# Kernel optimization log

Hardware: AMD Instinct MI355X
Metric: run time of the kernel (lower is better)

## Reference

```python
import jax, jax.numpy as jnp
import numpy as np

B, S, D = 1, 2048, 4096
H, KV = 32, 8
HD = D // H          # 128
N_REP = H // KV      # 4
ROPE_THETA = 10000.0


def setup_inputs() -> dict:
    key = jax.random.key(0)
    ks = jax.random.split(key, 5)
    x = jax.random.normal(ks[0], (B, S, D), dtype=jnp.float32)
    wq = jax.random.normal(ks[1], (H * HD, D), dtype=jnp.float32) * 0.02
    wk = jax.random.normal(ks[2], (KV * HD, D), dtype=jnp.float32) * 0.02
    wv = jax.random.normal(ks[3], (KV * HD, D), dtype=jnp.float32) * 0.02
    wo = jax.random.normal(ks[4], (D, H * HD), dtype=jnp.float32) * 0.02
    # precomputed RoPE frequencies: freqs_cis = exp(i * t * theta_j)
    inv_freq = 1.0 / (ROPE_THETA ** (np.arange(0, HD, 2, dtype=np.float32) / HD))  # [HD/2]
    angles = np.arange(S, dtype=np.float32)[:, None] * inv_freq[None, :]           # [S, HD/2]
    freqs_cos = jnp.asarray(np.cos(angles))
    freqs_sin = jnp.asarray(np.sin(angles))
    return {"x": x, "freqs_cos": freqs_cos, "freqs_sin": freqs_sin,
            "wq": wq, "wk": wk, "wv": wv, "wo": wo}


def _rope(t, cos, sin):
    # t: [B,S,h,HD]; even/odd interleaved pairs form complex numbers
    tr, ti = t[..., 0::2], t[..., 1::2]                 # [B,S,h,HD/2]
    cos = cos[None, :, None, :]
    sin = sin[None, :, None, :]
    out = jnp.stack([tr * cos - ti * sin, tr * sin + ti * cos], axis=-1)
    return out.reshape(t.shape)


def reference(x, freqs_cos, freqs_sin, wq, wk, wv, wo):
    bs, seqlen, _ = x.shape
    xq = jnp.einsum('bsd,ed->bse', x, wq).reshape(bs, seqlen, H, HD)
    xk = jnp.einsum('bsd,ed->bse', x, wk).reshape(bs, seqlen, KV, HD)
    xv = jnp.einsum('bsd,ed->bse', x, wv).reshape(bs, seqlen, KV, HD)
    xq = _rope(xq, freqs_cos, freqs_sin)
    xk = _rope(xk, freqs_cos, freqs_sin)
    # repeat_kv: GQA expand kv heads by n_rep
    keys = jnp.repeat(xk, N_REP, axis=2)    # [B,S,H,HD]
    values = jnp.repeat(xv, N_REP, axis=2)
    scale = 1.0 / np.sqrt(HD).astype(np.float32)
    scores = jnp.einsum('bshd,bthd->bhst', xq, keys) * scale  # [B,H,S,S]
    causal = jnp.tril(jnp.ones((seqlen, seqlen), dtype=bool))
    scores = jnp.where(causal[None, None], scores, jnp.finfo(scores.dtype).min)
    attn = jax.nn.softmax(scores, axis=-1)
    out = jnp.einsum('bhst,bthd->bshd', attn, values).reshape(bs, seqlen, H * HD)
    return jnp.einsum('bse,de->bsd', out, wo)
```

## Files before the change

### kernel.cpp

```cpp
#include <hip/hip_runtime.h>
#include <hip/hip_bf16.h>
#include <stdint.h>

#define SEQ   2048
#define DM    4096
#define NH    32
#define NKV   8
#define HD    128
#define DKV   1024

typedef __attribute__((ext_vector_type(8))) short bf8_t;
typedef __attribute__((ext_vector_type(4))) float f4_t;
typedef __attribute__((ext_vector_type(16))) float f16x;

__device__ __forceinline__ short f2bf(float f) {
  union { float f; uint32_t u; } v; v.f = f;
  uint32_t r = v.u + 0x7FFFu + ((v.u >> 16) & 1u);
  return (short)(r >> 16);
}
__device__ __forceinline__ float bf2f(short s) {
  union { uint32_t u; float f; } v; v.u = ((uint32_t)(uint16_t)s) << 16;
  return v.f;
}
__device__ __forceinline__ uint32_t cvtpk(float lo, float hi) {
  uint32_t r;
  asm("v_cvt_pk_bf16_f32 %0, %1, %2" : "=v"(r) : "v"(lo), "v"(hi));
  return r;
}

__device__ __forceinline__ void async_copy16(const void* gsrc, void* ldst) {
  auto g = reinterpret_cast<const __attribute__((address_space(1))) uint32_t*>(
      reinterpret_cast<uintptr_t>(gsrc));
  auto l = reinterpret_cast<__attribute__((address_space(3))) uint32_t*>(
      reinterpret_cast<uintptr_t>(ldst));
  __builtin_amdgcn_global_load_lds(g, l, 16, 0, 0);
}

__device__ __forceinline__ f4_t mfma16(bf8_t a, bf8_t b, f4_t c) {
  return __builtin_amdgcn_mfma_f32_16x16x32_bf16(a, b, c, 0, 0, 0);
}
__device__ __forceinline__ f16x mfma32(bf8_t a, bf8_t b, f16x c) {
  return __builtin_amdgcn_mfma_f32_32x32x16_bf16(a, b, c, 0, 0, 0);
}

template<int N> __device__ __forceinline__ void vmwait();
template<> __device__ __forceinline__ void vmwait<3>() {
  asm volatile("s_waitcnt vmcnt(3)" ::: "memory");
}
template<> __device__ __forceinline__ void vmwait<4>() {
  asm volatile("s_waitcnt vmcnt(4)" ::: "memory");
}

union U4B8 { uint32_t w[4]; bf8_t v; };

__global__ void cvt_all_kernel(const float* __restrict__ x,
                               const float* __restrict__ wq,
                               const float* __restrict__ wk,
                               const float* __restrict__ wv,
                               const float* __restrict__ wo,
                               short* __restrict__ out)
{
  const int E0 = SEQ * DM / 4;
  const int E1 = E0 + DM * DM / 4;
  const int E2 = E1 + DKV * DM / 4;
  const int E3 = E2 + DKV * DM / 4;
  const int E4 = E3 + DM * DM / 4;
  const int stride = gridDim.x * blockDim.x;
  for (int i = blockIdx.x * blockDim.x + threadIdx.x; i < E4; i += stride) {
    const float4* src; int off;
    if (i < E0)      { src = (const float4*)x;  off = i; }
    else if (i < E1) { src = (const float4*)wq; off = i - E0; }
    else if (i < E2) { src = (const float4*)wk; off = i - E1; }
    else if (i < E3) { src = (const float4*)wv; off = i - E2; }
    else             { src = (const float4*)wo; off = i - E3; }
    float4 v = src[off];
    short4 o;
    o.x = f2bf(v.x); o.y = f2bf(v.y); o.z = f2bf(v.z); o.w = f2bf(v.w);
    ((short4*)out)[i] = o;
  }
}

template<int MODE, int BM, int BN>
__global__ __launch_bounds__(512, 2)
void gemm8_kernel(const short* __restrict__ A,
                  const short* __restrict__ Bw,
                  float* __restrict__ Cf,
                  short* __restrict__ Cq,
                  short* __restrict__ Ck,
                  short* __restrict__ Cv)
{
  constexpr int MREP = BM / 32;
  constexpr int SB   = BN / 64;
  constexpr int SPP  = (SB == 4) ? 2 : (MREP / 4);
  constexpr int AJ   = BM / 128;
  constexpr int NT   = DM / 64;

  __shared__ short As[2][BM * 64];
  __shared__ short Bs[2][BN * 64];

  const int tid = threadIdx.x, lane = tid & 63, wid = tid >> 6;
  const int wr = wid >> 2, wn = wid & 3;
  const int cl = lane & 15, kh = lane >> 4;
  const int row0 = blockIdx.y * BM;
  const int col0 = blockIdx.x * BN;

  f4_t acc[MREP][SB];
  #pragma unroll
  for (int i = 0; i < MREP; i++)
    #pragma unroll
    for (int j = 0; j < SB; j++) { acc[i][j][0]=0.f; acc[i][j][1]=0.f; acc[i][j][2]=0.f; acc[i][j][3]=0.f; }

  auto STGA = [&](short* T, int h, int kt) {
    #pragma unroll
    for (int j = 0; j < AJ; ++j) {
      const int c = wid * (64 * AJ) + j * 64 + lane;
      const int row = h * (BM / 2) + (c >> 3), pcol = c & 7;
      const int lcol = pcol ^ (row & 7);
      async_copy16(&A[(size_t)(row0 + row) * DM + kt * 64 + lcol * 8],
                   &T[(h * (BM * 4) + c) * 8]);
    }
  };
  auto STGB = [&](short* T, int sl, int kt) {
    const int c = wid * 64 + lane;
    const int row = sl * 64 + (c >> 3), pcol = c & 7;
    const int lcol = pcol ^ (row & 7);
    async_copy16(&Bw[(size_t)(col0 + row) * DM + kt * 64 + lcol * 8],
                 &T[(sl * 512 + c) * 8]);
  };

  bf8_t bF[SB][2];
  bf8_t aF[SPP][2];
  auto LDA = [&](const short* T, int ms0) {
    #pragma unroll
    for (int s = 0; s < SPP; ++s)
      #pragma unroll
      for (int q = 0; q < 2; ++q) {
        const int row = wr * (BM / 2) + (ms0 + s) * 16 + cl;
        const int pcol = (q * 4 + kh) ^ (row & 7);
        aF[s][q] = *(const bf8_t*)&T[(row * 8 + pcol) * 8];
      }
  };
  auto LDB = [&](const short* T) {
    #pragma unroll
    for (int n = 0; n < SB; ++n)
      #pragma unroll
      for (int q = 0; q < 2; ++q) {
        const int row = wn * (16 * SB) + n * 16 + cl;
        const int pcol = (q * 4 + kh) ^ (row & 7);
        bF[n][q] = *(const bf8_t*)&T[(row * 8 + pcol) * 8];
      }
  };

#define PHASE(TA, TB, PH, READB, STGSTMT, VMC)                                \
  {                                                                           \
    LDA(TA, (PH) * SPP);                                                      \
    if (READB) LDB(TB);                                                       \
    STGSTMT                                                                   \
    __builtin_amdgcn_s_barrier();                                             \
    asm volatile("s_waitcnt lgkmcnt(0)" ::: "memory");                        \
    __builtin_amdgcn_s_setprio(1);                                            \
    _Pragma("unroll")                                                         \
    for (int s_ = 0; s_ < SPP; ++s_) {                                        \
      _Pragma("unroll")                                                       \
      for (int n_ = 0; n_ < SB; ++n_) {                                       \
        _Pragma("unroll")                                                     \
        for (int q_ = 0; q_ < 2; ++q_)                                        \
          acc[(PH) * SPP + s_][n_] =                                          \
              mfma16(aF[s_][q_], bF[n_][q_], acc[(PH) * SPP + s_][n_]);       \
      }                                                                       \
    }                                                                         \
    __builtin_amdgcn_s_setprio(0);                                            \
    if (VMC) vmwait<SB>();                                                    \
    __builtin_amdgcn_s_barrier();                                             \
  }

  #pragma unroll
  for (int sl = 0; sl < SB; ++sl) STGB(Bs[0], sl, 0);
  STGA(As[0], 0, 0); STGA(As[0], 1, 0);
  #pragma unroll
  for (int sl = 0; sl < SB; ++sl) STGB(Bs[1], sl, 1);
  vmwait<SB>();
  __builtin_amdgcn_s_barrier();

  for (int i = 0; i < NT / 2; ++i) {
    const int tA1 = 2 * i + 1;
    int t2 = 2 * i + 2; if (t2 > NT - 1) t2 = NT - 1;
    int t3 = 2 * i + 3; if (t3 > NT - 1) t3 = NT - 1;
    if constexpr (SB == 4) {
      PHASE(As[0], Bs[0], 0, true,  { STGA(As[1], 0, tA1); STGA(As[1], 1, tA1); }, false);
      PHASE(As[0], Bs[0], 1, false, { STGB(Bs[0], 0, t2); STGB(Bs[0], 1, t2);
                                      STGB(Bs[0], 2, t2); STGB(Bs[0], 3, t2); }, true);
      PHASE(As[1], Bs[1], 0, true,  { STGA(As[0], 0, t2); STGA(As[0], 1, t2); }, false);
      PHASE(As[1], Bs[1], 1, false, { STGB(Bs[1], 0, t3); STGB(Bs[1], 1, t3);
                                      STGB(Bs[1], 2, t3); STGB(Bs[1], 3, t3); }, true);
    } else {
      PHASE(As[0], Bs[0], 0, true,  { STGA(As[1], 0, tA1); STGA(As[1], 1, tA1); }, false);
      PHASE(As[0], Bs[0], 1, false, { STGB(Bs[0], 0, t2); }, false);
      PHASE(As[0], Bs[0], 2, false, { STGB(Bs[0], 1, t2); }, false);
      PHASE(As[0], Bs[0], 3, false, { STGB(Bs[0], 2, t2); }, true);
      PHASE(As[1], Bs[1], 0, true,  { STGA(As[0], 0, t2); STGA(As[0], 1, t2); }, false);
      PHASE(As[1], Bs[1], 1, false, { STGB(Bs[1], 0, t3); }, false);
      PHASE(As[1], Bs[1], 2, false, { STGB(Bs[1], 1, t3); }, false);
      PHASE(As[1], Bs[1], 3, false, { STGB(Bs[1], 2, t3); }, true);
    }
  }
#undef PHASE

  const int rb = kh * 4;
  #pragma unroll
  for (int mi = 0; mi < MREP; mi++) {
    const int m0 = row0 + wr * (BM / 2) + mi * 16 + rb;
    #pragma unroll
    for (int ni = 0; ni < SB; ni++) {
      const int n = col0 + wn * (16 * SB) + ni * 16 + cl;
      if (MODE == 0) {
        #pragma unroll
        for (int r = 0; r < 4; r++) Cf[(size_t)(m0 + r) * DM + n] = acc[mi][ni][r];
      } else if (n < DM) {
        #pragma unroll
        for (int r = 0; r < 4; r++) Cq[(size_t)(m0 + r) * DM + n] = f2bf(acc[mi][ni][r]);
      } else if (n < DM + DKV) {
        const int nk = n - DM;
        #pragma unroll
        for (int r = 0; r < 4; r++) Ck[(size_t)(m0 + r) * DKV + nk] = f2bf(acc[mi][ni][r]);
      } else {
        const int nv = n - DM - DKV;
        short4 pk;
        pk.x = f2bf(acc[mi][ni][0]); pk.y = f2bf(acc[mi][ni][1]);
        pk.z = f2bf(acc[mi][ni][2]); pk.w = f2bf(acc[mi][ni][3]);
        *(short4*)&Cv[(size_t)nv * SEQ + m0] = pk;
      }
    }
  }
}

__global__ void rope_kernel(short* __restrict__ Qb, short* __restrict__ Kb,
                            const float* __restrict__ fcos, const float* __restrict__ fsin)
{
  const int NQG = SEQ * (DM / 8);
  const int NKG = SEQ * (DKV / 8);
  int idx = blockIdx.x * blockDim.x + threadIdx.x;
  if (idx >= NQG + NKG) return;
  short* T; int s, g, row8;
  if (idx < NQG) { T = Qb; s = idx >> 9; g = idx & 511; row8 = DM / 8; }
  else { int j = idx - NQG; T = Kb; s = j >> 7; g = j & 127; row8 = DKV / 8; }
  const int i0 = (g & 15) * 4;
  const float4 cv = *(const float4*)&fcos[s * 64 + i0];
  const float4 sv = *(const float4*)&fsin[s * 64 + i0];
  short* ptr = T + (size_t)s * (row8 * 8) + g * 8;
  U4B8 v = *(U4B8*)ptr;
  U4B8 o;
  {
    const float e0 = bf2f((short)(v.w[0] & 0xFFFF)), o0 = bf2f((short)(v.w[0] >> 16));
    o.w[0] = cvtpk(e0 * cv.x - o0 * sv.x, e0 * sv.x + o0 * cv.x);
    const float e1 = bf2f((short)(v.w[1] & 0xFFFF)), o1 = bf2f((short)(v.w[1] >> 16));
    o.w[1] = cvtpk(e1 * cv.y - o1 * sv.y, e1 * sv.y + o1 * cv.y);
    const float e2 = bf2f((short)(v.w[2] & 0xFFFF)), o2 = bf2f((short)(v.w[2] >> 16));
    o.w[2] = cvtpk(e2 * cv.z - o2 * sv.z, e2 * sv.z + o2 * cv.z);
    const float e3 = bf2f((short)(v.w[3] & 0xFFFF)), o3 = bf2f((short)(v.w[3] >> 16));
    o.w[3] = cvtpk(e3 * cv.w - o3 * sv.w, e3 * sv.w + o3 * cv.w);
  }
  *(U4B8*)ptr = o;
}

__device__ __forceinline__ void flash_stage(const short* __restrict__ Kb,
                                            const short* __restrict__ Vt,
                                            short* Kl, short* Vl,
                                            int kv0, int hkv, int wid, int lane)
{
  #pragma unroll
  for (int i = 0; i < 4; ++i) {
    int c = wid * 256 + i * 64 + lane;
    int row = c >> 4, pos = c & 15;
    int dc = pos ^ (row & 7);
    async_copy16(&Kb[(size_t)(kv0 + row) * DKV + hkv * HD + dc * 8], &Kl[c * 8]);
  }
  #pragma unroll
  for (int i = 0; i < 4; ++i) {
    int c = wid * 256 + i * 64 + lane;
    int row = c >> 3, pos = c & 7;
    int kc = pos ^ (row & 7);
    async_copy16(&Vt[(size_t)(hkv * HD + row) * SEQ + kv0 + kc * 8], &Vl[c * 8]);
  }
}

__device__ __forceinline__ void flash_compute(const short* __restrict__ Kl,
                                              const short* __restrict__ Vl,
                                              const bf8_t* qF, f16x* accO,
                                              float& m_run, float& l_run,
                                              int kv0, int qw0, int c31, int hi)
{
  const float scale = 0.08838834764831845f;

  f16x accS[2];
  #pragma unroll
  for (int nu = 0; nu < 2; ++nu) {
    #pragma unroll
    for (int r = 0; r < 16; ++r) accS[nu][r] = 0.f;
  }
  #pragma unroll
  for (int nu = 0; nu < 2; ++nu) {
    const int row = nu * 32 + c31, rx = row & 7;
    #pragma unroll
    for (int s = 0; s < 8; ++s) {
      const int pos = (2 * s + hi) ^ rx;
      bf8_t kf = *(const bf8_t*)&Kl[row * 128 + pos * 8];
      accS[nu] = mfma32(kf, qF[s], accS[nu]);
    }
  }

  if (kv0 + 63 > qw0) {
    const int q_abs = qw0 + c31;
    #pragma unroll
    for (int nu = 0; nu < 2; ++nu)
      #pragma unroll
      for (int r = 0; r < 16; ++r) {
        const int kv_abs = kv0 + 32 * nu + (r & 3) + 8 * (r >> 2) + 4 * hi;
        if (kv_abs > q_abs) accS[nu][r] = -3.0e38f;
      }
  }

  float rm = -3.0e38f;
  #pragma unroll
  for (int nu = 0; nu < 2; ++nu)
    #pragma unroll
    for (int r = 0; r < 16; ++r) rm = fmaxf(rm, accS[nu][r]);
  rm = fmaxf(rm, __shfl_xor(rm, 32));
  const float pmax = rm * scale;
  if (!__all(pmax - m_run <= 8.0f)) {
    const float mnew = fmaxf(m_run, pmax);
    const float corr = __expf(m_run - mnew);
    m_run = mnew;
    l_run *= corr;
    #pragma unroll
    for (int dt = 0; dt < 4; ++dt)
      #pragma unroll
      for (int r = 0; r < 16; ++r) accO[dt][r] *= corr;
  }

  float tsum = 0.f;
  uint32_t u[8][2];
  #pragma unroll
  for (int m = 0; m < 8; ++m) {
    const int nu = m >> 2, rb = 4 * (m & 3);
    float p0 = __expf(fmaf(accS[nu][rb + 0], scale, -m_run));
    float p1 = __expf(fmaf(accS[nu][rb + 1], scale, -m_run));
    float p2 = __expf(fmaf(accS[nu][rb + 2], scale, -m_run));
    float p3 = __expf(fmaf(accS[nu][rb + 3], scale, -m_run));
    tsum += (p0 + p1) + (p2 + p3);
    u[m][0] = cvtpk(p0, p1);
    u[m][1] = cvtpk(p2, p3);
  }
  l_run += tsum + __shfl_xor(tsum, 32);

  bf8_t pa[4];
  #pragma unroll
  for (int ks = 0; ks < 4; ++ks) {
    const uint32_t a0 = u[2 * ks][0],     a1 = u[2 * ks][1];
    const uint32_t b0 = u[2 * ks + 1][0], b1 = u[2 * ks + 1][1];
    const uint32_t mp0 = hi ? a0 : b0, mp1 = hi ? a1 : b1;
    const uint32_t s0 = __shfl_xor(mp0, 32), s1 = __shfl_xor(mp1, 32);
    U4B8 f;
    f.w[0] = hi ? s0 : a0;
    f.w[1] = hi ? s1 : a1;
    f.w[2] = hi ? b0 : s0;
    f.w[3] = hi ? b1 : s1;
    pa[ks] = f.v;
  }

  #pragma unroll
  for (int dt = 0; dt < 4; ++dt) {
    const int row = dt * 32 + c31, rx = row & 7;
    #pragma unroll
    for (int ks = 0; ks < 4; ++ks) {
      const int pos = (2 * ks + hi) ^ rx;
      bf8_t vf = *(const bf8_t*)&Vl[row * 64 + pos * 8];
      accO[dt] = mfma32(vf, pa[ks], accO[dt]);
    }
  }
}

__global__ __launch_bounds__(256, 2)
void flash_kernel(const short* __restrict__ Qb,
                  const short* __restrict__ Kb,
                  const short* __restrict__ Vt,
                  short* __restrict__ Ob)
{
  __shared__ short Kl0[64 * 128], Kl1[64 * 128];
  __shared__ short Vl0[128 * 64], Vl1[128 * 64];

  const int tid = threadIdx.x, lane = tid & 63, wid = tid >> 6;
  const int c31 = lane & 31, hi = lane >> 5;

  const int b = blockIdx.x;
  const int pairid = b & 255, halfsel = b >> 8;
  const int h = pairid >> 3, p = pairid & 7;
  const int qt = halfsel ? (15 - p) : p;
  const int q0 = qt * 128;
  const int hkv = h >> 2;
  const int qw0 = q0 + wid * 32;

  bf8_t qF[8];
  {
    const size_t qb = (size_t)(qw0 + c31) * DM + h * HD + hi * 8;
    #pragma unroll
    for (int s = 0; s < 8; ++s) qF[s] = *(const bf8_t*)&Qb[qb + s * 16];
  }

  f16x accO[4];
  #pragma unroll
  for (int dt = 0; dt < 4; ++dt)
    #pragma unroll
    for (int r = 0; r < 16; ++r) accO[dt][r] = 0.f;
  float m_run = -INFINITY, l_run = 0.f;

  const int nt = (q0 >> 6) + 2;

  flash_stage(Kb, Vt, Kl0, Vl0, 0, hkv, wid, lane);
  __syncthreads();
  for (int t = 0; t < nt; t += 2) {
    flash_stage(Kb, Vt, Kl1, Vl1, (t + 1) * 64, hkv, wid, lane);
    if (t * 64 <= qw0 + 31)
      flash_compute(Kl0, Vl0, qF, accO, m_run, l_run, t * 64, qw0, c31, hi);
    __syncthreads();
    if (t + 2 < nt) flash_stage(Kb, Vt, Kl0, Vl0, (t + 2) * 64, hkv, wid, lane);
    if ((t + 1) * 64 <= qw0 + 31)
      flash_compute(Kl1, Vl1, qF, accO, m_run, l_run, (t + 1) * 64, qw0, c31, hi);
    __syncthreads();
  }

  short* Ol = (wid < 2) ? &Kl0[wid * 4096] : &Kl1[(wid - 2) * 4096];
  const float oinv = 1.0f / l_run;
  #pragma unroll
  for (int dt = 0; dt < 4; ++dt)
    #pragma unroll
    for (int w = 0; w < 8; ++w) {
      const int r = 2 * w;
      const int d0 = (r & 3) + 8 * (r >> 2) + 4 * hi + dt * 32;
      const uint32_t pk = cvtpk(accO[dt][r] * oinv, accO[dt][r + 1] * oinv);
      const int pos = (d0 >> 3) ^ (c31 & 7);
      *(uint32_t*)&Ol[c31 * 128 + pos * 8 + (d0 & 7)] = pk;
    }
  __syncthreads();
  const int rowq = lane >> 1;
  #pragma unroll
  for (int i = 0; i < 8; ++i) {
    const int dc = (lane & 1) * 8 + i;
    const int pos = dc ^ (rowq & 7);
    int4 v = *(const int4*)&Ol[rowq * 128 + pos * 8];
    *(int4*)&Ob[(size_t)(q0 + wid * 32 + rowq) * DM + h * HD + dc * 8] = v;
  }
}

extern "C" void kernel_launch(void* const* d_in, const int* in_sizes, int n_in,
                              void* d_out, int out_size, void* d_ws, size_t ws_size,
                              hipStream_t stream)
{
  const float* x    = (const float*)d_in[0];
  const float* fcos = (const float*)d_in[1];
  const float* fsin = (const float*)d_in[2];
  const float* wq   = (const float*)d_in[3];
  const float* wk   = (const float*)d_in[4];
  const float* wv   = (const float*)d_in[5];
  const float* wo   = (const float*)d_in[6];
  float* out = (float*)d_out;

  char* p = (char*)d_ws;
  short* xb  = (short*)p; p += (size_t)SEQ * DM * 2;
  short* wqb = (short*)p; p += (size_t)DM * DM * 2;
  short* wkb = (short*)p; p += (size_t)DKV * DM * 2;
  short* wvb = (short*)p; p += (size_t)DKV * DM * 2;
  short* wob = (short*)p; p += (size_t)DM * DM * 2;
  short* Qb  = (short*)p; p += (size_t)SEQ * DM * 2;
  short* Kb  = (short*)p; p += (size_t)SEQ * DKV * 2;
  short* Vt  = (short*)p; p += (size_t)DKV * SEQ * 2;
  short* Ab  = (short*)p; p += (size_t)SEQ * DM * 2;
  (void)wkb; (void)wvb;

  cvt_all_kernel<<<2048, 256, 0, stream>>>(x, wq, wk, wv, wo, xb);

  gemm8_kernel<1, 256, 192><<<dim3(32, 8), 512, 0, stream>>>(xb, wqb,
                                                             nullptr, Qb, Kb, Vt);
  rope_kernel<<<5120, 256, 0, stream>>>(Qb, Kb, fcos, fsin);
  flash_kernel<<<512, 256, 0, stream>>>(Qb, Kb, Vt, Ab);
  gemm8_kernel<0, 128, 256><<<dim3(16, 16), 512, 0, stream>>>(Ab, wob,
                                                              out, nullptr, nullptr, nullptr);
}
```

Before: 275.9 us.

## Fuse Q RoPE into flash Q-fragment load and simplify GEMM phase schedule

The flash kernel now applies RoPE to Q as it loads the Q fragments into registers, reading cos/sin directly. The standalone rope kernel shrinks to handle K only, which removes a full read and write pass over the Q buffer. Separately, the GEMM main loop is unified to two compute phases per buffer with SPP = MREP/2. For the QKV GEMM configuration (BN=192) this halves the number of phases and barriers but puts more MFMAs and loads in each phase, which may hurt load/compute interleaving.

```diff
diff --git a/kernel.cpp b/kernel.cpp
--- a/kernel.cpp
+++ b/kernel.cpp
@@ -91,7 +91,7 @@
 {
   constexpr int MREP = BM / 32;
   constexpr int SB   = BN / 64;
-  constexpr int SPP  = (SB == 4) ? 2 : (MREP / 4);
+  constexpr int SPP  = MREP / 2;
   constexpr int AJ   = BM / 128;
   constexpr int NT   = DM / 64;
 
@@ -183,26 +183,17 @@
   __builtin_amdgcn_s_barrier();
 
   for (int i = 0; i < NT / 2; ++i) {
-    const int tA1 = 2 * i + 1;
+    const int t1 = 2 * i + 1;
     int t2 = 2 * i + 2; if (t2 > NT - 1) t2 = NT - 1;
     int t3 = 2 * i + 3; if (t3 > NT - 1) t3 = NT - 1;
-    if constexpr (SB == 4) {
-      PHASE(As[0], Bs[0], 0, true,  { STGA(As[1], 0, tA1); STGA(As[1], 1, tA1); }, false);
-      PHASE(As[0], Bs[0], 1, false, { STGB(Bs[0], 0, t2); STGB(Bs[0], 1, t2);
-                                      STGB(Bs[0], 2, t2); STGB(Bs[0], 3, t2); }, true);
-      PHASE(As[1], Bs[1], 0, true,  { STGA(As[0], 0, t2); STGA(As[0], 1, t2); }, false);
-      PHASE(As[1], Bs[1], 1, false, { STGB(Bs[1], 0, t3); STGB(Bs[1], 1, t3);
-                                      STGB(Bs[1], 2, t3); STGB(Bs[1], 3, t3); }, true);
-    } else {
-      PHASE(As[0], Bs[0], 0, true,  { STGA(As[1], 0, tA1); STGA(As[1], 1, tA1); }, false);
-      PHASE(As[0], Bs[0], 1, false, { STGB(Bs[0], 0, t2); }, false);
-      PHASE(As[0], Bs[0], 2, false, { STGB(Bs[0], 1, t2); }, false);
-      PHASE(As[0], Bs[0], 3, false, { STGB(Bs[0], 2, t2); }, true);
-      PHASE(As[1], Bs[1], 0, true,  { STGA(As[0], 0, t2); STGA(As[0], 1, t2); }, false);
-      PHASE(As[1], Bs[1], 1, false, { STGB(Bs[1], 0, t3); }, false);
-      PHASE(As[1], Bs[1], 2, false, { STGB(Bs[1], 1, t3); }, false);
-      PHASE(As[1], Bs[1], 3, false, { STGB(Bs[1], 2, t3); }, true);
-    }
+    PHASE(As[0], Bs[0], 0, true,
+          { STGA(As[1], 0, t1); STGA(As[1], 1, t1); }, false);
+    PHASE(As[0], Bs[0], 1, false,
+          { _Pragma("unroll") for (int sl = 0; sl < SB; ++sl) STGB(Bs[0], sl, t2); }, true);
+    PHASE(As[1], Bs[1], 0, true,
+          { STGA(As[0], 0, t2); STGA(As[0], 1, t2); }, false);
+    PHASE(As[1], Bs[1], 1, false,
+          { _Pragma("unroll") for (int sl = 0; sl < SB; ++sl) STGB(Bs[1], sl, t3); }, true);
   }
 #undef PHASE
 
@@ -234,20 +225,17 @@
   }
 }
 
-__global__ void rope_kernel(short* __restrict__ Qb, short* __restrict__ Kb,
-                            const float* __restrict__ fcos, const float* __restrict__ fsin)
-{
-  const int NQG = SEQ * (DM / 8);
+__global__ void rope_k_kernel(short* __restrict__ Kb,
+                              const float* __restrict__ fcos, const float* __restrict__ fsin)
+{
   const int NKG = SEQ * (DKV / 8);
   int idx = blockIdx.x * blockDim.x + threadIdx.x;
-  if (idx >= NQG + NKG) return;
-  short* T; int s, g, row8;
-  if (idx < NQG) { T = Qb; s = idx >> 9; g = idx & 511; row8 = DM / 8; }
-  else { int j = idx - NQG; T = Kb; s = j >> 7; g = j & 127; row8 = DKV / 8; }
+  if (idx >= NKG) return;
+  const int s = idx >> 7, g = idx & 127;
   const int i0 = (g & 15) * 4;
   const float4 cv = *(const float4*)&fcos[s * 64 + i0];
   const float4 sv = *(const float4*)&fsin[s * 64 + i0];
-  short* ptr = T + (size_t)s * (row8 * 8) + g * 8;
+  short* ptr = Kb + (size_t)s * DKV + g * 8;
   U4B8 v = *(U4B8*)ptr;
   U4B8 o;
   {
@@ -384,6 +372,8 @@
 void flash_kernel(const short* __restrict__ Qb,
                   const short* __restrict__ Kb,
                   const short* __restrict__ Vt,
+                  const float* __restrict__ fcos,
+                  const float* __restrict__ fsin,
                   short* __restrict__ Ob)
 {
   __shared__ short Kl0[64 * 128], Kl1[64 * 128];
@@ -402,9 +392,27 @@
 
   bf8_t qF[8];
   {
-    const size_t qb = (size_t)(qw0 + c31) * DM + h * HD + hi * 8;
-    #pragma unroll
-    for (int s = 0; s < 8; ++s) qF[s] = *(const bf8_t*)&Qb[qb + s * 16];
+    const int qrow = qw0 + c31;
+    const size_t qb = (size_t)qrow * DM + h * HD + hi * 8;
+    const int tb = qrow * 64 + hi * 4;
+    #pragma unroll
+    for (int s = 0; s < 8; ++s) {
+      U4B8 v; v.v = *(const bf8_t*)&Qb[qb + s * 16];
+      const float4 cv = *(const float4*)&fcos[tb + s * 8];
+      const float4 sv = *(const float4*)&fsin[tb + s * 8];
+      U4B8 o;
+      {
+        const float e0 = bf2f((short)(v.w[0] & 0xFFFF)), d0 = bf2f((short)(v.w[0] >> 16));
+        o.w[0] = cvtpk(e0 * cv.x - d0 * sv.x, e0 * sv.x + d0 * cv.x);
+        const float e1 = bf2f((short)(v.w[1] & 0xFFFF)), d1 = bf2f((short)(v.w[1] >> 16));
+        o.w[1] = cvtpk(e1 * cv.y - d1 * sv.y, e1 * sv.y + d1 * cv.y);
+        const float e2 = bf2f((short)(v.w[2] & 0xFFFF)), d2 = bf2f((short)(v.w[2] >> 16));
+        o.w[2] = cvtpk(e2 * cv.z - d2 * sv.z, e2 * sv.z + d2 * cv.z);
+        const float e3 = bf2f((short)(v.w[3] & 0xFFFF)), d3 = bf2f((short)(v.w[3] >> 16));
+        o.w[3] = cvtpk(e3 * cv.w - d3 * sv.w, e3 * sv.w + d3 * cv.w);
+      }
+      qF[s] = o.v;
+    }
   }
 
   f16x accO[4];
@@ -481,8 +489,8 @@
 
   gemm8_kernel<1, 256, 192><<<dim3(32, 8), 512, 0, stream>>>(xb, wqb,
                                                              nullptr, Qb, Kb, Vt);
-  rope_kernel<<<5120, 256, 0, stream>>>(Qb, Kb, fcos, fsin);
-  flash_kernel<<<512, 256, 0, stream>>>(Qb, Kb, Vt, Ab);
+  rope_k_kernel<<<1024, 256, 0, stream>>>(Kb, fcos, fsin);
+  flash_kernel<<<512, 256, 0, stream>>>(Qb, Kb, Vt, fcos, fsin, Ab);
   gemm8_kernel<0, 128, 256><<<dim3(16, 16), 512, 0, stream>>>(Ab, wob,
                                                               out, nullptr, nullptr, nullptr);
 }
```

Result: no change. 275.8 us, median of 3 (-0.0%).
